# Kernel optimization log

Hardware: AMD Instinct MI355X
Metric: run time of the kernel (lower is better)

## Reference

```python
import jax, jax.numpy as jnp
import numpy as np

B, T, TC, C, CC, H = 2, 2048, 512, 1024, 512, 16
D = C // H  # head dim = 64


def setup_inputs() -> dict:
    key = jax.random.key(0)
    ks = jax.random.split(key, 18)
    w = lambda k, i, o: (jax.random.normal(k, (i, o), jnp.float32) / np.sqrt(i).astype(np.float32))
    return {
        "x": jax.random.normal(ks[0], (B, T, C), jnp.float32),
        "cross_input": jax.random.normal(ks[1], (B, TC, CC), jnp.float32),
        "Wk": w(ks[2], C, C),  "bk": jnp.zeros((C,), jnp.float32),
        "Wq": w(ks[3], C, C),  "bq": jnp.zeros((C,), jnp.float32),
        "Wv": w(ks[4], C, C),  "bv": jnp.zeros((C,), jnp.float32),
        "Wck": w(ks[5], CC, C), "bck": jnp.zeros((C,), jnp.float32),
        "Wcq": w(ks[6], C, C),  "bcq": jnp.zeros((C,), jnp.float32),
        "Wcv": w(ks[7], CC, C), "bcv": jnp.zeros((C,), jnp.float32),
        "Wp": w(ks[8], C, C),   "bp": jnp.zeros((C,), jnp.float32),
    }


def _heads(t):
    # [B, L, C] -> [B, H, L, D]
    b, l, _ = t.shape
    return t.reshape(b, l, H, D).transpose(0, 2, 1, 3)


def reference(x, cross_input, Wk, bk, Wq, bq, Wv, bv, Wck, bck, Wcq, bcq, Wcv, bcv, Wp, bp):
    scale = np.float32(1.0 / np.sqrt(D))
    q = _heads(x @ Wq + bq)
    k = _heads(x @ Wk + bk)
    v = _heads(x @ Wv + bv)
    # causal self-attention with materialized scores (faithful to original)
    att = jnp.einsum("bhqd,bhkd->bhqk", q, k) * scale
    causal = jnp.tril(jnp.ones((T, T), bool))
    att = jnp.where(causal[None, None], att, -jnp.inf)
    y = jnp.einsum("bhqk,bhkd->bhqd", jax.nn.softmax(att, axis=-1), v)
    # cross-attention (no mask)
    qc = _heads(x @ Wcq + bcq)
    kc = _heads(cross_input @ Wck + bck)
    vc = _heads(cross_input @ Wcv + bcv)
    attc = jnp.einsum("bhqd,bhkd->bhqk", qc, kc) * scale
    y = y + jnp.einsum("bhqk,bhkd->bhqd", jax.nn.softmax(attc, axis=-1), vc)
    # merge heads + output projection (dropout prob = 0 -> identity)
    y = y.transpose(0, 2, 1, 3).reshape(x.shape[0], T, C)
    return y @ Wp + bp
```

## Files before the change

### kernel.cpp

```cpp
#include <hip/hip_runtime.h>
#include <hip/hip_bf16.h>
#include <type_traits>

typedef __bf16 bf16;
typedef __bf16 bf16x8 __attribute__((ext_vector_type(8)));
typedef float floatx4 __attribute__((ext_vector_type(4)));
typedef unsigned int uint32x4 __attribute__((ext_vector_type(4)));

#if __has_builtin(__builtin_amdgcn_exp2f)
#define EXP2(x) __builtin_amdgcn_exp2f(x)
#else
#define EXP2(x) exp2f(x)
#endif

__device__ __forceinline__ void glds16(const bf16* g, bf16* l) {
  __builtin_amdgcn_global_load_lds((const __attribute__((address_space(1))) void*)g,
                                   (__attribute__((address_space(3))) void*)l, 16, 0, 0);
}

__device__ __forceinline__ unsigned pack_bf16(float a, float b) {
  unsigned short ua = __builtin_bit_cast(unsigned short, (bf16)a);
  unsigned short ub = __builtin_bit_cast(unsigned short, (bf16)b);
  return (unsigned)ua | ((unsigned)ub << 16);
}

struct PrepArgs {
  const float* x; const float* xc;
  bf16* xbf; bf16* xcbf;
  const float* b4[4];
  const float* bc[2];
  float* bias4; float* biasc;
  const float* W[7];
  bf16* WT[7];
};

__global__ __launch_bounds__(256) void prep_kernel(PrepArgs a) {
  __shared__ bf16 tsh[32][33];
  const int bx = blockIdx.x, tid = threadIdx.x;
  if (bx < 4096) {
    int i = bx * 256 + tid;
    float4 f = ((const float4*)a.x)[i];
    bf16 t[4] = {(bf16)f.x, (bf16)f.y, (bf16)f.z, (bf16)f.w};
    *(uint2*)&a.xbf[(long)i * 4] = *(const uint2*)t;
  } else if (bx < 4608) {
    int i = (bx - 4096) * 256 + tid;
    float4 f = ((const float4*)a.xc)[i];
    bf16 t[4] = {(bf16)f.x, (bf16)f.y, (bf16)f.z, (bf16)f.w};
    *(uint2*)&a.xcbf[(long)i * 4] = *(const uint2*)t;
  } else if (bx < 4632) {
    int lb = bx - 4608;
    if (lb < 16) {
      int i = lb * 256 + tid;
      int sec = i >> 10;
      float v = a.b4[sec][i & 1023];
      if (sec == 0 || sec == 3) v *= 0.18033688f;
      a.bias4[i] = v;
    } else {
      int i = (lb - 16) * 256 + tid;
      a.biasc[i] = a.bc[i >> 10][i & 1023];
    }
  } else {
    int t = bx - 4632, w, R, bxw, byw;
    if (t < 5120) { w = t >> 10; R = 1024; int l = t & 1023; bxw = l & 31; byw = l >> 5; }
    else { int t2 = t - 5120; w = 5 + (t2 >> 9); R = 512; int l = t2 & 511; bxw = l & 31; byw = l >> 5; }
    const float* in = a.W[w];
    bf16* out = a.WT[w];
    const float sc = (w == 0 || w == 3) ? 0.18033688f : 1.0f;
    int tx = tid & 31, ty = tid >> 5;
    int c = bxw * 32 + tx;
#pragma unroll
    for (int i = 0; i < 4; i++) {
      int r = byw * 32 + ty + i * 8;
      tsh[ty + i * 8][tx] = (bf16)(in[(long)r * 1024 + c] * sc);
    }
    __syncthreads();
    int oc = byw * 32 + tx;
#pragma unroll
    for (int i = 0; i < 4; i++) {
      int orr = bxw * 32 + ty + i * 8;
      out[(long)orr * R + oc] = tsh[tx][ty + i * 8];
    }
  }
}

template <typename OutT>
__global__ __launch_bounds__(256, 3) void gemm128(const bf16* __restrict__ A,
                                                  const bf16* __restrict__ Bt,
                                                  const float* __restrict__ bias,
                                                  OutT* __restrict__ C,
                                                  int M, int N, int K, int ldc,
                                                  bf16* __restrict__ Vt,
                                                  int vcol0, int vcol1, int Lt, int tok_shift) {
  __shared__ alignas(16) bf16 As[128 * 32];
  __shared__ alignas(16) bf16 Bs[128 * 32];
  const int tid = threadIdx.x, wave = tid >> 6, lane = tid & 63;
  const int l16 = lane & 15, l4 = lane >> 4;
  const int wm = wave & 1, wn = wave >> 1;
  const int n0 = blockIdx.x * 128, m0 = blockIdx.y * 128;
  const int lrow = lane >> 2, lch = (lane & 3) * 8;

  floatx4 acc[4][4];
#pragma unroll
  for (int mt = 0; mt < 4; mt++)
#pragma unroll
    for (int nt = 0; nt < 4; nt++) acc[mt][nt] = (floatx4){0.f, 0.f, 0.f, 0.f};

  const bf16* Ag = A + (long)(m0 + wave * 32 + lrow) * K + lch;
  const bf16* Bg = Bt + (long)(n0 + wave * 32 + lrow) * K + lch;
  bf16* Al = &As[(wave * 32) * 32];
  bf16* Bl = &Bs[(wave * 32) * 32];

  for (int k0 = 0; k0 < K; k0 += 32) {
    __syncthreads();
    glds16(Ag + k0, Al);
    glds16(Ag + k0 + (long)16 * K, Al + 16 * 32);
    glds16(Bg + k0, Bl);
    glds16(Bg + k0 + (long)16 * K, Bl + 16 * 32);
    __syncthreads();
    bf16x8 a[4], b[4];
#pragma unroll
    for (int mt = 0; mt < 4; mt++) a[mt] = *(const bf16x8*)&As[(wm * 64 + mt * 16 + l16) * 32 + l4 * 8];
#pragma unroll
    for (int nt = 0; nt < 4; nt++) b[nt] = *(const bf16x8*)&Bs[(wn * 64 + nt * 16 + l16) * 32 + l4 * 8];
#pragma unroll
    for (int mt = 0; mt < 4; mt++)
#pragma unroll
      for (int nt = 0; nt < 4; nt++)
        acc[mt][nt] = __builtin_amdgcn_mfma_f32_16x16x32_bf16(a[mt], b[nt], acc[mt][nt], 0, 0, 0);
  }

  const bool vpath = (vcol0 >= 0) && (n0 >= vcol0) && (n0 < vcol1);
  if (!vpath) {
    const int coladj = (vcol0 >= 0 && n0 >= vcol1) ? (vcol1 - vcol0) : 0;
#pragma unroll
    for (int nt = 0; nt < 4; nt++) {
      int col = n0 + wn * 64 + nt * 16 + l16;
      float bv = bias[col];
#pragma unroll
      for (int mt = 0; mt < 4; mt++)
#pragma unroll
        for (int r = 0; r < 4; r++) {
          int row = m0 + wm * 64 + mt * 16 + l4 * 4 + r;
          float v = acc[mt][nt][r] + bv;
          if constexpr (std::is_same_v<OutT, float>) C[(long)row * ldc + col - coladj] = v;
          else                                       C[(long)row * ldc + col - coladj] = (bf16)v;
        }
    }
  } else {
#pragma unroll
    for (int nt = 0; nt < 4; nt++) {
      int col = n0 + wn * 64 + nt * 16 + l16;
      int c = col - vcol0, hh = c >> 6, dd = c & 63;
      float bv = bias[col];
#pragma unroll
      for (int mt = 0; mt < 4; mt++) {
        int t0 = m0 + wm * 64 + mt * 16 + l4 * 4;
        int bb = t0 >> tok_shift, t = t0 & ((1 << tok_shift) - 1);
        t = (t & ~31) | (((t >> 2) & 3) << 3) | (((t >> 4) & 1) << 2) | (t & 3);
        bf16 tmp[4];
#pragma unroll
        for (int r = 0; r < 4; r++) tmp[r] = (bf16)(acc[mt][nt][r] + bv);
        *(uint2*)&Vt[(((long)bb * 16 + hh) * 64 + dd) * Lt + t] = *(const uint2*)tmp;
      }
    }
  }
}

__global__ __launch_bounds__(256, 2) void attn_kernel(const bf16* __restrict__ QKQc,
                                                      const bf16* __restrict__ VtB,
                                                      const bf16* __restrict__ KcB,
                                                      const bf16* __restrict__ VctB,
                                                      bf16* __restrict__ Y) {
  __shared__ float Lbuf[4][4][16];
  __shared__ alignas(16) bf16 U[4 * 64 * 72];
  __shared__ alignas(16) float Osave[256][20];
  const int tid = threadIdx.x, w = tid >> 6, lane = tid & 63;
  const int l16 = lane & 15, l4 = lane >> 4;
  const int bh = blockIdx.x, h = bh & 15, b = bh >> 4;
  const int qt = 31 - (int)blockIdx.y;
  const int q0 = qt * 64;
  const int wk = w * 32;
  const float NEG = -1e30f;

  for (int phase = 0; phase < 2; phase++) {
    const bf16 *Qb, *Kb, *Vtb;
    int kstr, vtstr, nkt;
    if (phase == 0) {
      Qb = QKQc + (long)b * 2048 * 3072 + h * 64;
      Kb = Qb + 1024;                              kstr = 3072;
      Vtb = VtB + ((long)b * 16 + h) * 64 * 2048;  vtstr = 2048;
      nkt = (qt + 2) >> 1;
    } else {
      Qb = QKQc + (long)b * 2048 * 3072 + h * 64 + 2048;
      Kb = KcB + (long)b * 512 * 1024 + h * 64;    kstr = 1024;
      Vtb = VctB + ((long)b * 16 + h) * 64 * 512;  vtstr = 512;
      nkt = 4;
    }

    __syncthreads();

    bf16x8 qf[4][2];
#pragma unroll
    for (int qtt = 0; qtt < 4; qtt++) {
      const bf16* qp = Qb + (long)(q0 + qtt * 16 + l16) * 3072 + l4 * 8;
#pragma unroll
      for (int ds = 0; ds < 2; ds++) qf[qtt][ds] = *(const bf16x8*)(qp + ds * 32);
    }

    float l_i[4];
#pragma unroll
    for (int qtt = 0; qtt < 4; qtt++) l_i[qtt] = 0.f;
    floatx4 oacc[4][4];
#pragma unroll
    for (int mtd = 0; mtd < 4; mtd++)
#pragma unroll
      for (int qtt = 0; qtt < 4; qtt++) oacc[mtd][qtt] = (floatx4){0.f, 0.f, 0.f, 0.f};

    bf16x8 kreg[2][2];
#pragma unroll
    for (int mt = 0; mt < 2; mt++)
#pragma unroll
      for (int ds = 0; ds < 2; ds++)
        kreg[mt][ds] = *(const bf16x8*)(Kb + (long)(wk + mt * 16 + l16) * kstr + ds * 32 + l4 * 8);

    floatx4 sacc[2][4];
#pragma unroll
    for (int mt = 0; mt < 2; mt++)
#pragma unroll
      for (int qtt = 0; qtt < 4; qtt++) sacc[mt][qtt] = (floatx4){0.f, 0.f, 0.f, 0.f};
#pragma unroll
    for (int ds = 0; ds < 2; ds++)
#pragma unroll
      for (int mt = 0; mt < 2; mt++)
#pragma unroll
        for (int qtt = 0; qtt < 4; qtt++)
          sacc[mt][qtt] = __builtin_amdgcn_mfma_f32_16x16x32_bf16(kreg[mt][ds], qf[qtt][ds], sacc[mt][qtt], 0, 0, 0);

    for (int kt = 0; kt < nkt; kt++) {
      const int kbase = kt * 128 + wk;
      const bool more = (kt + 1 < nkt);

      bf16x8 vc[4];
#pragma unroll
      for (int mtd = 0; mtd < 4; mtd++)
        vc[mtd] = *(const bf16x8*)(Vtb + (long)(mtd * 16 + l16) * vtstr + kbase + l4 * 8);

      if (more) {
        const int nb = kbase + 128;
#pragma unroll
        for (int mt = 0; mt < 2; mt++)
#pragma unroll
          for (int ds = 0; ds < 2; ds++)
            kreg[mt][ds] = *(const bf16x8*)(Kb + (long)(nb + mt * 16 + l16) * kstr + ds * 32 + l4 * 8);
      }

      if (phase == 0 && kt == nkt - 1) {
#pragma unroll
        for (int mt = 0; mt < 2; mt++) {
          int keyb = kbase + mt * 16 + l4 * 4;
#pragma unroll
          for (int qtt = 0; qtt < 4; qtt++) {
            int q = q0 + qtt * 16 + l16;
#pragma unroll
            for (int r = 0; r < 4; r++)
              if (keyb + r > q) sacc[mt][qtt][r] = NEG;
          }
        }
      }

#pragma unroll
      for (int qtt = 0; qtt < 4; qtt++) {
        float p0 = EXP2(sacc[0][qtt][0]), p1 = EXP2(sacc[0][qtt][1]);
        float p2 = EXP2(sacc[0][qtt][2]), p3 = EXP2(sacc[0][qtt][3]);
        float p4 = EXP2(sacc[1][qtt][0]), p5 = EXP2(sacc[1][qtt][1]);
        float p6 = EXP2(sacc[1][qtt][2]), p7 = EXP2(sacc[1][qtt][3]);
        l_i[qtt] += ((p0 + p1) + (p2 + p3)) + ((p4 + p5) + (p6 + p7));
        uint32x4 pu = {pack_bf16(p0, p1), pack_bf16(p2, p3), pack_bf16(p4, p5), pack_bf16(p6, p7)};
        bf16x8 pf = __builtin_bit_cast(bf16x8, pu);
        __builtin_amdgcn_s_setprio(1);
#pragma unroll
        for (int mtd = 0; mtd < 4; mtd++)
          oacc[mtd][qtt] = __builtin_amdgcn_mfma_f32_16x16x32_bf16(vc[mtd], pf, oacc[mtd][qtt], 0, 0, 0);
        __builtin_amdgcn_s_setprio(0);
      }

      if (more) {
#pragma unroll
        for (int mt = 0; mt < 2; mt++)
#pragma unroll
          for (int qtt = 0; qtt < 4; qtt++) sacc[mt][qtt] = (floatx4){0.f, 0.f, 0.f, 0.f};
        __builtin_amdgcn_s_setprio(1);
#pragma unroll
        for (int ds = 0; ds < 2; ds++)
#pragma unroll
          for (int mt = 0; mt < 2; mt++)
#pragma unroll
            for (int qtt = 0; qtt < 4; qtt++)
              sacc[mt][qtt] = __builtin_amdgcn_mfma_f32_16x16x32_bf16(kreg[mt][ds], qf[qtt][ds], sacc[mt][qtt], 0, 0, 0);
        __builtin_amdgcn_s_setprio(0);
      }
    }

    float lsum[4];
#pragma unroll
    for (int qtt = 0; qtt < 4; qtt++) {
      float r = l_i[qtt];
      r += __shfl_xor(r, 16);
      r += __shfl_xor(r, 32);
      lsum[qtt] = r;
    }
    if (l4 == 0) {
#pragma unroll
      for (int qtt = 0; qtt < 4; qtt++) Lbuf[w][qtt][l16] = lsum[qtt];
    }
    __syncthreads();
    float denom = 0.f;
#pragma unroll
    for (int s = 0; s < 4; s++) denom += Lbuf[s][w][l16];
#pragma unroll
    for (int qtt = 0; qtt < 4; qtt++)
#pragma unroll
      for (int mtd = 0; mtd < 4; mtd++) {
        uint2 u = {pack_bf16(oacc[mtd][qtt][0], oacc[mtd][qtt][1]),
                   pack_bf16(oacc[mtd][qtt][2], oacc[mtd][qtt][3])};
        *(uint2*)&U[((w * 64) + qtt * 16 + l16) * 72 + mtd * 16 + l4 * 4] = u;
      }
    __syncthreads();
    float sum[16];
#pragma unroll
    for (int j = 0; j < 16; j++) sum[j] = 0.f;
#pragma unroll
    for (int s = 0; s < 4; s++) {
      bf16x8 c0 = *(const bf16x8*)&U[((s * 64) + w * 16 + l16) * 72 + l4 * 16];
      bf16x8 c1 = *(const bf16x8*)&U[((s * 64) + w * 16 + l16) * 72 + l4 * 16 + 8];
#pragma unroll
      for (int j = 0; j < 8; j++) { sum[j] += (float)c0[j]; sum[8 + j] += (float)c1[j]; }
    }
    float invd = 1.0f / denom;
    if (phase == 0) {
#pragma unroll
      for (int jj = 0; jj < 4; jj++) {
        float4 v = {sum[jj * 4] * invd, sum[jj * 4 + 1] * invd,
                    sum[jj * 4 + 2] * invd, sum[jj * 4 + 3] * invd};
        *(float4*)&Osave[tid][jj * 4] = v;
      }
    } else {
      long row = (long)b * 2048 + q0 + w * 16 + l16;
      bf16 out[16];
#pragma unroll
      for (int jj = 0; jj < 4; jj++) {
        float4 v = *(const float4*)&Osave[tid][jj * 4];
        out[jj * 4]     = (bf16)(v.x + sum[jj * 4] * invd);
        out[jj * 4 + 1] = (bf16)(v.y + sum[jj * 4 + 1] * invd);
        out[jj * 4 + 2] = (bf16)(v.z + sum[jj * 4 + 2] * invd);
        out[jj * 4 + 3] = (bf16)(v.w + sum[jj * 4 + 3] * invd);
      }
      *(bf16x8*)&Y[row * 1024 + h * 64 + l4 * 16] = *(const bf16x8*)&out[0];
      *(bf16x8*)&Y[row * 1024 + h * 64 + l4 * 16 + 8] = *(const bf16x8*)&out[8];
    }
  }
}

extern "C" void kernel_launch(void* const* d_in, const int* in_sizes, int n_in,
                              void* d_out, int out_size, void* d_ws, size_t ws_size,
                              hipStream_t stream) {
  const float* x   = (const float*)d_in[0];
  const float* xc  = (const float*)d_in[1];
  const float* Wk  = (const float*)d_in[2];  const float* bk  = (const float*)d_in[3];
  const float* Wq  = (const float*)d_in[4];  const float* bq  = (const float*)d_in[5];
  const float* Wv  = (const float*)d_in[6];  const float* bv  = (const float*)d_in[7];
  const float* Wck = (const float*)d_in[8];  const float* bck = (const float*)d_in[9];
  const float* Wcq = (const float*)d_in[10]; const float* bcq = (const float*)d_in[11];
  const float* Wcv = (const float*)d_in[12]; const float* bcv = (const float*)d_in[13];
  const float* Wp  = (const float*)d_in[14]; const float* bp  = (const float*)d_in[15];

  char* ws = (char*)d_ws;
  const size_t MB = 1ull << 20;
  bf16*  WT_all = (bf16*)(ws + 0);
  bf16*  WC_all = (bf16*)(ws + 8 * MB);
  bf16*  WpT    = (bf16*)(ws + 10 * MB);
  bf16*  xbf    = (bf16*)(ws + 12 * MB);
  bf16*  Yb     = xbf;
  bf16*  xcbf   = (bf16*)(ws + 20 * MB);
  float* bias4  = (float*)(ws + 21 * MB);
  float* biasc  = (float*)(ws + 21 * MB + 65536);
  bf16*  QKQc   = (bf16*)(ws + 22 * MB);
  bf16*  VtB    = (bf16*)(ws + 46 * MB);
  bf16*  KcB    = (bf16*)(ws + 54 * MB);
  bf16*  VctB   = (bf16*)(ws + 56 * MB);

  PrepArgs pa;
  pa.x = x; pa.xc = xc; pa.xbf = xbf; pa.xcbf = xcbf;
  pa.b4[0] = bq; pa.b4[1] = bk; pa.b4[2] = bv; pa.b4[3] = bcq;
  pa.bc[0] = bck; pa.bc[1] = bcv;
  pa.bias4 = bias4; pa.biasc = biasc;
  pa.W[0] = Wq;  pa.WT[0] = WT_all + 0ll * 1024 * 1024;
  pa.W[1] = Wk;  pa.WT[1] = WT_all + 1ll * 1024 * 1024;
  pa.W[2] = Wv;  pa.WT[2] = WT_all + 2ll * 1024 * 1024;
  pa.W[3] = Wcq; pa.WT[3] = WT_all + 3ll * 1024 * 1024;
  pa.W[4] = Wp;  pa.WT[4] = WpT;
  pa.W[5] = Wck; pa.WT[5] = WC_all + 0ll * 1024 * 512;
  pa.W[6] = Wcv; pa.WT[6] = WC_all + 1ll * 1024 * 512;
  prep_kernel<<<10776, 256, 0, stream>>>(pa);

  gemm128<bf16><<<dim3(32, 32), 256, 0, stream>>>(xbf, WT_all, bias4, QKQc,
                                                  4096, 4096, 1024, 3072,
                                                  VtB, 2048, 3072, 2048, 11);
  gemm128<bf16><<<dim3(16, 8), 256, 0, stream>>>(xcbf, WC_all, biasc, KcB,
                                                 1024, 2048, 512, 1024,
                                                 VctB, 1024, 2048, 512, 9);

  attn_kernel<<<dim3(32, 32), 256, 0, stream>>>(QKQc, VtB, KcB, VctB, Yb);

  gemm128<float><<<dim3(8, 32), 256, 0, stream>>>(Yb, WpT, bp, (float*)d_out,
                                                  4096, 1024, 1024, 1024,
                                                  nullptr, -1, -1, 0, 0);
}
```

Before: 255.6 us.

## Pair causal q-tiles per block, stage V via async LDS loads, swizzle GEMM grid

The attention kernel now processes two query tiles per block (qt and 31-qt), which balances causal work and halves the grid. V tiles are fetched with double-buffered global_load_lds into a swizzled per-wave LDS buffer, with explicit vmcnt waits, instead of direct global loads. The cross-wave output reduction is split into two passes over a smaller LDS buffer to cut shared-memory use. The GEMM blocks also get an XCD-aware remapping of workgroup IDs. Together these aim to reduce load imbalance and latency stalls, at the cost of more LDS use, hand-written waitcnt fragility and fewer blocks in flight.

```diff
diff --git a/kernel.cpp b/kernel.cpp
--- a/kernel.cpp
+++ b/kernel.cpp
@@ -96,7 +96,10 @@
   const int tid = threadIdx.x, wave = tid >> 6, lane = tid & 63;
   const int l16 = lane & 15, l4 = lane >> 4;
   const int wm = wave & 1, wn = wave >> 1;
-  const int n0 = blockIdx.x * 128, m0 = blockIdx.y * 128;
+  const int nwg = gridDim.x * gridDim.y;
+  int lin = blockIdx.y * gridDim.x + blockIdx.x;
+  lin = (lin & 7) * (nwg >> 3) + (lin >> 3);
+  const int n0 = (lin % gridDim.x) * 128, m0 = (lin / gridDim.x) * 128;
   const int lrow = lane >> 2, lch = (lane & 3) * 8;
 
   floatx4 acc[4][4];
@@ -172,191 +175,224 @@
                                                       const bf16* __restrict__ VctB,
                                                       bf16* __restrict__ Y) {
   __shared__ float Lbuf[4][4][16];
-  __shared__ alignas(16) bf16 U[4 * 64 * 72];
+  __shared__ alignas(16) bf16 U2[4 * 64 * 40];
   __shared__ alignas(16) float Osave[256][20];
+  __shared__ alignas(16) bf16 Vsl[4][2][2048];
   const int tid = threadIdx.x, w = tid >> 6, lane = tid & 63;
   const int l16 = lane & 15, l4 = lane >> 4;
   const int bh = blockIdx.x, h = bh & 15, b = bh >> 4;
-  const int qt = 31 - (int)blockIdx.y;
-  const int q0 = qt * 64;
   const int wk = w * 32;
   const float NEG = -1e30f;
-
-  for (int phase = 0; phase < 2; phase++) {
-    const bf16 *Qb, *Kb, *Vtb;
-    int kstr, vtstr, nkt;
-    if (phase == 0) {
-      Qb = QKQc + (long)b * 2048 * 3072 + h * 64;
-      Kb = Qb + 1024;                              kstr = 3072;
-      Vtb = VtB + ((long)b * 16 + h) * 64 * 2048;  vtstr = 2048;
-      nkt = (qt + 2) >> 1;
-    } else {
-      Qb = QKQc + (long)b * 2048 * 3072 + h * 64 + 2048;
-      Kb = KcB + (long)b * 512 * 1024 + h * 64;    kstr = 1024;
-      Vtb = VctB + ((long)b * 16 + h) * 64 * 512;  vtstr = 512;
-      nkt = 4;
-    }
-
-    __syncthreads();
-
-    bf16x8 qf[4][2];
-#pragma unroll
-    for (int qtt = 0; qtt < 4; qtt++) {
-      const bf16* qp = Qb + (long)(q0 + qtt * 16 + l16) * 3072 + l4 * 8;
-#pragma unroll
-      for (int ds = 0; ds < 2; ds++) qf[qtt][ds] = *(const bf16x8*)(qp + ds * 32);
-    }
-
-    float l_i[4];
-#pragma unroll
-    for (int qtt = 0; qtt < 4; qtt++) l_i[qtt] = 0.f;
-    floatx4 oacc[4][4];
-#pragma unroll
-    for (int mtd = 0; mtd < 4; mtd++)
-#pragma unroll
-      for (int qtt = 0; qtt < 4; qtt++) oacc[mtd][qtt] = (floatx4){0.f, 0.f, 0.f, 0.f};
-
-    bf16x8 kreg[2][2];
-#pragma unroll
-    for (int mt = 0; mt < 2; mt++)
+  const int swv = (l4 ^ ((l16 >> 1) & 3)) * 8;
+
+  for (int qi = 0; qi < 2; qi++) {
+    const int qt = qi ? (int)blockIdx.y : 31 - (int)blockIdx.y;
+    const int q0 = qt * 64;
+
+    for (int phase = 0; phase < 2; phase++) {
+      const bf16 *Qb, *Kb, *Vtb;
+      int kstr, vtstr, nkt;
+      if (phase == 0) {
+        Qb = QKQc + (long)b * 2048 * 3072 + h * 64;
+        Kb = Qb + 1024;                              kstr = 3072;
+        Vtb = VtB + ((long)b * 16 + h) * 64 * 2048;  vtstr = 2048;
+        nkt = (qt + 2) >> 1;
+      } else {
+        Qb = QKQc + (long)b * 2048 * 3072 + h * 64 + 2048;
+        Kb = KcB + (long)b * 512 * 1024 + h * 64;    kstr = 1024;
+        Vtb = VctB + ((long)b * 16 + h) * 64 * 512;  vtstr = 512;
+        nkt = 4;
+      }
+
+      __syncthreads();
+
+      bf16x8 qf[4][2];
+#pragma unroll
+      for (int qtt = 0; qtt < 4; qtt++) {
+        const bf16* qp = Qb + (long)(q0 + qtt * 16 + l16) * 3072 + l4 * 8;
+#pragma unroll
+        for (int ds = 0; ds < 2; ds++) qf[qtt][ds] = *(const bf16x8*)(qp + ds * 32);
+      }
+
+      float l_i[4];
+#pragma unroll
+      for (int qtt = 0; qtt < 4; qtt++) l_i[qtt] = 0.f;
+      floatx4 oacc[4][4];
+#pragma unroll
+      for (int mtd = 0; mtd < 4; mtd++)
+#pragma unroll
+        for (int qtt = 0; qtt < 4; qtt++) oacc[mtd][qtt] = (floatx4){0.f, 0.f, 0.f, 0.f};
+
+      bf16x8 kreg[2][2];
+#pragma unroll
+      for (int mt = 0; mt < 2; mt++)
+#pragma unroll
+        for (int ds = 0; ds < 2; ds++)
+          kreg[mt][ds] = *(const bf16x8*)(Kb + (long)(wk + mt * 16 + l16) * kstr + ds * 32 + l4 * 8);
+#pragma unroll
+      for (int i = 0; i < 4; i++) {
+        int c = i * 64 + lane, r = c >> 2;
+        int kc = ((c & 3) ^ ((r >> 1) & 3)) * 8;
+        glds16(Vtb + (long)r * vtstr + wk + kc, &Vsl[w][0][i * 512]);
+      }
+
+      floatx4 sacc[2][4];
+#pragma unroll
+      for (int mt = 0; mt < 2; mt++)
+#pragma unroll
+        for (int qtt = 0; qtt < 4; qtt++) sacc[mt][qtt] = (floatx4){0.f, 0.f, 0.f, 0.f};
 #pragma unroll
       for (int ds = 0; ds < 2; ds++)
-        kreg[mt][ds] = *(const bf16x8*)(Kb + (long)(wk + mt * 16 + l16) * kstr + ds * 32 + l4 * 8);
-
-    floatx4 sacc[2][4];
-#pragma unroll
-    for (int mt = 0; mt < 2; mt++)
-#pragma unroll
-      for (int qtt = 0; qtt < 4; qtt++) sacc[mt][qtt] = (floatx4){0.f, 0.f, 0.f, 0.f};
-#pragma unroll
-    for (int ds = 0; ds < 2; ds++)
-#pragma unroll
-      for (int mt = 0; mt < 2; mt++)
+#pragma unroll
+        for (int mt = 0; mt < 2; mt++)
+#pragma unroll
+          for (int qtt = 0; qtt < 4; qtt++)
+            sacc[mt][qtt] = __builtin_amdgcn_mfma_f32_16x16x32_bf16(kreg[mt][ds], qf[qtt][ds], sacc[mt][qtt], 0, 0, 0);
+
+      for (int kt = 0; kt < nkt; kt++) {
+        const int kbase = kt * 128 + wk;
+        const bool more = (kt + 1 < nkt);
+
+        if (more) {
+          bf16* dst = &Vsl[w][(kt + 1) & 1][0];
+          const int nb = kbase + 128;
+#pragma unroll
+          for (int i = 0; i < 4; i++) {
+            int c = i * 64 + lane, r = c >> 2;
+            int kc = ((c & 3) ^ ((r >> 1) & 3)) * 8;
+            glds16(Vtb + (long)r * vtstr + nb + kc, dst + i * 512);
+          }
+        }
+
+        if (phase == 0 && kt == nkt - 1) {
+#pragma unroll
+          for (int mt = 0; mt < 2; mt++) {
+            int keyb = kbase + mt * 16 + l4 * 4;
+#pragma unroll
+            for (int qtt = 0; qtt < 4; qtt++) {
+              int q = q0 + qtt * 16 + l16;
+#pragma unroll
+              for (int r = 0; r < 4; r++)
+                if (keyb + r > q) sacc[mt][qtt][r] = NEG;
+            }
+          }
+        }
+
+        bf16x8 vc[4];
+        {
+          const bf16* sl = &Vsl[w][kt & 1][0];
+          if (more) asm volatile("s_waitcnt vmcnt(4)" ::: "memory");
+          else      asm volatile("s_waitcnt vmcnt(0)" ::: "memory");
+#pragma unroll
+          for (int mtd = 0; mtd < 4; mtd++)
+            vc[mtd] = *(const bf16x8*)&sl[(mtd * 16 + l16) * 32 + swv];
+        }
+
+        if (more) {
+          const int nb = kbase + 128;
+#pragma unroll
+          for (int mt = 0; mt < 2; mt++)
+#pragma unroll
+            for (int ds = 0; ds < 2; ds++)
+              kreg[mt][ds] = *(const bf16x8*)(Kb + (long)(nb + mt * 16 + l16) * kstr + ds * 32 + l4 * 8);
+        }
+
+#pragma unroll
+        for (int qtt = 0; qtt < 4; qtt++) {
+          float p0 = EXP2(sacc[0][qtt][0]), p1 = EXP2(sacc[0][qtt][1]);
+          float p2 = EXP2(sacc[0][qtt][2]), p3 = EXP2(sacc[0][qtt][3]);
+          float p4 = EXP2(sacc[1][qtt][0]), p5 = EXP2(sacc[1][qtt][1]);
+          float p6 = EXP2(sacc[1][qtt][2]), p7 = EXP2(sacc[1][qtt][3]);
+          l_i[qtt] += ((p0 + p1) + (p2 + p3)) + ((p4 + p5) + (p6 + p7));
+          uint32x4 pu = {pack_bf16(p0, p1), pack_bf16(p2, p3), pack_bf16(p4, p5), pack_bf16(p6, p7)};
+          bf16x8 pf = __builtin_bit_cast(bf16x8, pu);
+          __builtin_amdgcn_s_setprio(1);
+#pragma unroll
+          for (int mtd = 0; mtd < 4; mtd++)
+            oacc[mtd][qtt] = __builtin_amdgcn_mfma_f32_16x16x32_bf16(vc[mtd], pf, oacc[mtd][qtt], 0, 0, 0);
+          __builtin_amdgcn_s_setprio(0);
+        }
+
+        if (more) {
+#pragma unroll
+          for (int mt = 0; mt < 2; mt++)
+#pragma unroll
+            for (int qtt = 0; qtt < 4; qtt++) sacc[mt][qtt] = (floatx4){0.f, 0.f, 0.f, 0.f};
+          __builtin_amdgcn_s_setprio(1);
+#pragma unroll
+          for (int ds = 0; ds < 2; ds++)
+#pragma unroll
+            for (int mt = 0; mt < 2; mt++)
+#pragma unroll
+              for (int qtt = 0; qtt < 4; qtt++)
+                sacc[mt][qtt] = __builtin_amdgcn_mfma_f32_16x16x32_bf16(kreg[mt][ds], qf[qtt][ds], sacc[mt][qtt], 0, 0, 0);
+          __builtin_amdgcn_s_setprio(0);
+        }
+      }
+
+      float lsum[4];
+#pragma unroll
+      for (int qtt = 0; qtt < 4; qtt++) {
+        float r = l_i[qtt];
+        r += __shfl_xor(r, 16);
+        r += __shfl_xor(r, 32);
+        lsum[qtt] = r;
+      }
+      if (l4 == 0) {
+#pragma unroll
+        for (int qtt = 0; qtt < 4; qtt++) Lbuf[w][qtt][l16] = lsum[qtt];
+      }
+      float sum[16];
+#pragma unroll
+      for (int j = 0; j < 16; j++) sum[j] = 0.f;
+      float denom = 0.f;
+#pragma unroll
+      for (int p = 0; p < 2; p++) {
+        __syncthreads();
 #pragma unroll
         for (int qtt = 0; qtt < 4; qtt++)
-          sacc[mt][qtt] = __builtin_amdgcn_mfma_f32_16x16x32_bf16(kreg[mt][ds], qf[qtt][ds], sacc[mt][qtt], 0, 0, 0);
-
-    for (int kt = 0; kt < nkt; kt++) {
-      const int kbase = kt * 128 + wk;
-      const bool more = (kt + 1 < nkt);
-
-      bf16x8 vc[4];
-#pragma unroll
-      for (int mtd = 0; mtd < 4; mtd++)
-        vc[mtd] = *(const bf16x8*)(Vtb + (long)(mtd * 16 + l16) * vtstr + kbase + l4 * 8);
-
-      if (more) {
-        const int nb = kbase + 128;
-#pragma unroll
-        for (int mt = 0; mt < 2; mt++)
-#pragma unroll
-          for (int ds = 0; ds < 2; ds++)
-            kreg[mt][ds] = *(const bf16x8*)(Kb + (long)(nb + mt * 16 + l16) * kstr + ds * 32 + l4 * 8);
-      }
-
-      if (phase == 0 && kt == nkt - 1) {
-#pragma unroll
-        for (int mt = 0; mt < 2; mt++) {
-          int keyb = kbase + mt * 16 + l4 * 4;
-#pragma unroll
-          for (int qtt = 0; qtt < 4; qtt++) {
-            int q = q0 + qtt * 16 + l16;
-#pragma unroll
-            for (int r = 0; r < 4; r++)
-              if (keyb + r > q) sacc[mt][qtt][r] = NEG;
+#pragma unroll
+          for (int mm = 0; mm < 2; mm++) {
+            int mtd = p * 2 + mm;
+            uint2 u = {pack_bf16(oacc[mtd][qtt][0], oacc[mtd][qtt][1]),
+                       pack_bf16(oacc[mtd][qtt][2], oacc[mtd][qtt][3])};
+            *(uint2*)&U2[((w * 64) + qtt * 16 + l16) * 40 + mm * 16 + l4 * 4] = u;
           }
-        }
-      }
-
-#pragma unroll
-      for (int qtt = 0; qtt < 4; qtt++) {
-        float p0 = EXP2(sacc[0][qtt][0]), p1 = EXP2(sacc[0][qtt][1]);
-        float p2 = EXP2(sacc[0][qtt][2]), p3 = EXP2(sacc[0][qtt][3]);
-        float p4 = EXP2(sacc[1][qtt][0]), p5 = EXP2(sacc[1][qtt][1]);
-        float p6 = EXP2(sacc[1][qtt][2]), p7 = EXP2(sacc[1][qtt][3]);
-        l_i[qtt] += ((p0 + p1) + (p2 + p3)) + ((p4 + p5) + (p6 + p7));
-        uint32x4 pu = {pack_bf16(p0, p1), pack_bf16(p2, p3), pack_bf16(p4, p5), pack_bf16(p6, p7)};
-        bf16x8 pf = __builtin_bit_cast(bf16x8, pu);
-        __builtin_amdgcn_s_setprio(1);
-#pragma unroll
-        for (int mtd = 0; mtd < 4; mtd++)
-          oacc[mtd][qtt] = __builtin_amdgcn_mfma_f32_16x16x32_bf16(vc[mtd], pf, oacc[mtd][qtt], 0, 0, 0);
-        __builtin_amdgcn_s_setprio(0);
-      }
-
-      if (more) {
-#pragma unroll
-        for (int mt = 0; mt < 2; mt++)
-#pragma unroll
-          for (int qtt = 0; qtt < 4; qtt++) sacc[mt][qtt] = (floatx4){0.f, 0.f, 0.f, 0.f};
-        __builtin_amdgcn_s_setprio(1);
-#pragma unroll
-        for (int ds = 0; ds < 2; ds++)
-#pragma unroll
-          for (int mt = 0; mt < 2; mt++)
-#pragma unroll
-            for (int qtt = 0; qtt < 4; qtt++)
-              sacc[mt][qtt] = __builtin_amdgcn_mfma_f32_16x16x32_bf16(kreg[mt][ds], qf[qtt][ds], sacc[mt][qtt], 0, 0, 0);
-        __builtin_amdgcn_s_setprio(0);
-      }
-    }
-
-    float lsum[4];
-#pragma unroll
-    for (int qtt = 0; qtt < 4; qtt++) {
-      float r = l_i[qtt];
-      r += __shfl_xor(r, 16);
-      r += __shfl_xor(r, 32);
-      lsum[qtt] = r;
-    }
-    if (l4 == 0) {
-#pragma unroll
-      for (int qtt = 0; qtt < 4; qtt++) Lbuf[w][qtt][l16] = lsum[qtt];
-    }
-    __syncthreads();
-    float denom = 0.f;
-#pragma unroll
-    for (int s = 0; s < 4; s++) denom += Lbuf[s][w][l16];
-#pragma unroll
-    for (int qtt = 0; qtt < 4; qtt++)
-#pragma unroll
-      for (int mtd = 0; mtd < 4; mtd++) {
-        uint2 u = {pack_bf16(oacc[mtd][qtt][0], oacc[mtd][qtt][1]),
-                   pack_bf16(oacc[mtd][qtt][2], oacc[mtd][qtt][3])};
-        *(uint2*)&U[((w * 64) + qtt * 16 + l16) * 72 + mtd * 16 + l4 * 4] = u;
-      }
-    __syncthreads();
-    float sum[16];
-#pragma unroll
-    for (int j = 0; j < 16; j++) sum[j] = 0.f;
-#pragma unroll
-    for (int s = 0; s < 4; s++) {
-      bf16x8 c0 = *(const bf16x8*)&U[((s * 64) + w * 16 + l16) * 72 + l4 * 16];
-      bf16x8 c1 = *(const bf16x8*)&U[((s * 64) + w * 16 + l16) * 72 + l4 * 16 + 8];
-#pragma unroll
-      for (int j = 0; j < 8; j++) { sum[j] += (float)c0[j]; sum[8 + j] += (float)c1[j]; }
-    }
-    float invd = 1.0f / denom;
-    if (phase == 0) {
-#pragma unroll
-      for (int jj = 0; jj < 4; jj++) {
-        float4 v = {sum[jj * 4] * invd, sum[jj * 4 + 1] * invd,
-                    sum[jj * 4 + 2] * invd, sum[jj * 4 + 3] * invd};
-        *(float4*)&Osave[tid][jj * 4] = v;
-      }
-    } else {
-      long row = (long)b * 2048 + q0 + w * 16 + l16;
-      bf16 out[16];
-#pragma unroll
-      for (int jj = 0; jj < 4; jj++) {
-        float4 v = *(const float4*)&Osave[tid][jj * 4];
-        out[jj * 4]     = (bf16)(v.x + sum[jj * 4] * invd);
-        out[jj * 4 + 1] = (bf16)(v.y + sum[jj * 4 + 1] * invd);
-        out[jj * 4 + 2] = (bf16)(v.z + sum[jj * 4 + 2] * invd);
-        out[jj * 4 + 3] = (bf16)(v.w + sum[jj * 4 + 3] * invd);
-      }
-      *(bf16x8*)&Y[row * 1024 + h * 64 + l4 * 16] = *(const bf16x8*)&out[0];
-      *(bf16x8*)&Y[row * 1024 + h * 64 + l4 * 16 + 8] = *(const bf16x8*)&out[8];
+        __syncthreads();
+        if (p == 0)
+          denom = Lbuf[0][w][l16] + Lbuf[1][w][l16] + Lbuf[2][w][l16] + Lbuf[3][w][l16];
+        if ((l4 >> 1) == p) {
+#pragma unroll
+          for (int s = 0; s < 4; s++) {
+            bf16x8 c0 = *(const bf16x8*)&U2[((s * 64) + w * 16 + l16) * 40 + (l4 & 1) * 16];
+            bf16x8 c1 = *(const bf16x8*)&U2[((s * 64) + w * 16 + l16) * 40 + (l4 & 1) * 16 + 8];
+#pragma unroll
+            for (int j = 0; j < 8; j++) { sum[j] += (float)c0[j]; sum[8 + j] += (float)c1[j]; }
+          }
+        }
+      }
+      float invd = 1.0f / denom;
+      if (phase == 0) {
+#pragma unroll
+        for (int jj = 0; jj < 4; jj++) {
+          float4 v = {sum[jj * 4] * invd, sum[jj * 4 + 1] * invd,
+                      sum[jj * 4 + 2] * invd, sum[jj * 4 + 3] * invd};
+          *(float4*)&Osave[tid][jj * 4] = v;
+        }
+      } else {
+        long row = (long)b * 2048 + q0 + w * 16 + l16;
+        bf16 out[16];
+#pragma unroll
+        for (int jj = 0; jj < 4; jj++) {
+          float4 v = *(const float4*)&Osave[tid][jj * 4];
+          out[jj * 4]     = (bf16)(v.x + sum[jj * 4] * invd);
+          out[jj * 4 + 1] = (bf16)(v.y + sum[jj * 4 + 1] * invd);
+          out[jj * 4 + 2] = (bf16)(v.z + sum[jj * 4 + 2] * invd);
+          out[jj * 4 + 3] = (bf16)(v.w + sum[jj * 4 + 3] * invd);
+        }
+        *(bf16x8*)&Y[row * 1024 + h * 64 + l4 * 16] = *(const bf16x8*)&out[0];
+        *(bf16x8*)&Y[row * 1024 + h * 64 + l4 * 16 + 8] = *(const bf16x8*)&out[8];
+      }
     }
   }
 }
@@ -410,7 +446,7 @@
                                                  1024, 2048, 512, 1024,
                                                  VctB, 1024, 2048, 512, 9);
 
-  attn_kernel<<<dim3(32, 32), 256, 0, stream>>>(QKQc, VtB, KcB, VctB, Yb);
+  attn_kernel<<<dim3(32, 16), 256, 0, stream>>>(QKQc, VtB, KcB, VctB, Yb);
 
   gemm128<float><<<dim3(8, 32), 256, 0, stream>>>(Yb, WpT, bp, (float*)d_out,
                                                   4096, 1024, 1024, 1024,
```

Result: faster. 246.3 us (-3.6%).
